# Optimization experiments

Hardware: AMD Instinct MI355X
Metric: run time of the kernel (lower is better)

The kernel has to match this reference:

```python
import jax, jax.numpy as jnp
import numpy as np

BITS = 4
GROUPSIZE = 128
IN_FEATURES = 4096
OUT_FEATURES = 11008
PACK = 32 // BITS  # 8 nibbles per int32
MASK = (1 << BITS) - 1


def setup_inputs() -> dict:
    key = jax.random.key(0)
    k1, k2, k3, k4, k5 = jax.random.split(key, 5)
    x = jax.random.normal(k1, (4, 2048, IN_FEATURES), dtype=jnp.float32)
    qweight = jax.random.randint(k2, (IN_FEATURES // 32 * BITS, OUT_FEATURES), 0, 2147483647, dtype=jnp.int32)
    n_groups = IN_FEATURES // GROUPSIZE  # 32
    qzeros = jax.random.randint(k3, (n_groups, OUT_FEATURES // 32 * BITS), 0, 2147483647, dtype=jnp.int32)
    scales = jax.random.uniform(k4, (n_groups, OUT_FEATURES), dtype=jnp.float32) * 0.01 + 1e-3
    bias = jax.random.normal(k5, (OUT_FEATURES,), dtype=jnp.float32)
    return {"x": x, "qweight": qweight, "qzeros": qzeros, "scales": scales, "bias": bias}


def _dequant(qweight, qzeros, scales):
    # GPTQ 4-bit unpack + group-wise dequant (g_idx=None / non-act-order path).
    shifts = jnp.arange(0, 32, BITS, dtype=jnp.int32)  # [8]
    # zero points: (G, out//8) int32 -> (G, out)
    z = ((qzeros[:, :, None] >> shifts[None, None, :]) & MASK)
    z = z.reshape(qzeros.shape[0], -1).astype(scales.dtype)  # (G, out)
    # weights: (in//8, out) int32 -> (in//8, 8, out) -> (G, groupsize, out)
    w = ((qweight[:, None, :] >> shifts[None, :, None]) & MASK).astype(scales.dtype)
    n_groups = scales.shape[0]
    w = w.reshape(n_groups, GROUPSIZE, -1)
    # W = scale * q - scale * zero, per group
    W = scales[:, None, :] * w - (z * scales)[:, None, :]
    return W.reshape(IN_FEATURES, OUT_FEATURES)


def reference(x, qweight, qzeros, scales, bias):
    W = _dequant(qweight, qzeros, scales)  # (in, out) fp32
    return jnp.matmul(x, W) + bias
```

## Files before the change

kernel.cpp:

```cpp
#include <hip/hip_runtime.h>
#include <hip/hip_bf16.h>
#include <stdint.h>

#define M_DIM 8192
#define K_DIM 4096
#define N_DIM 11008

typedef int i32x4 __attribute__((ext_vector_type(4)));
typedef float f32x4 __attribute__((ext_vector_type(4)));

typedef __attribute__((address_space(1))) const void global_cvoid;
typedef __attribute__((address_space(3))) void lds_void;

__device__ __forceinline__ void gload_lds16(const void* g, void* l) {
  __builtin_amdgcn_global_load_lds((global_cvoid*)g, (lds_void*)l, 16, 0, 0);
}

__global__ void k_prep(const float* __restrict__ x, signed char* __restrict__ xq,
                       float* __restrict__ sx, const int* __restrict__ qw,
                       const int* __restrict__ qz, signed char* __restrict__ wt) {
  if (blockIdx.x < M_DIM) {
    int m = blockIdx.x;
    int tx = threadIdx.x;
    const float4* row = (const float4*)(x + (size_t)m * K_DIM);
    float4 v[4];
    float mx = 0.f;
    #pragma unroll
    for (int i = 0; i < 4; ++i) {
      v[i] = row[tx * 4 + i];
      mx = fmaxf(mx, fmaxf(fmaxf(fabsf(v[i].x), fabsf(v[i].y)),
                           fmaxf(fabsf(v[i].z), fabsf(v[i].w))));
    }
    #pragma unroll
    for (int off = 1; off < 64; off <<= 1)
      mx = fmaxf(mx, __shfl_xor(mx, off));
    __shared__ float wmx[4];
    if ((tx & 63) == 0) wmx[tx >> 6] = mx;
    __syncthreads();
    mx = fmaxf(fmaxf(wmx[0], wmx[1]), fmaxf(wmx[2], wmx[3]));
    mx = fmaxf(mx, 1e-20f);
    float scale = 127.0f / mx;
    if (tx == 0) sx[m] = mx / 127.0f;
    union { signed char c[16]; uint4 u; } p;
    #pragma unroll
    for (int i = 0; i < 4; ++i) {
      p.c[i * 4 + 0] = (signed char)(int)rintf(v[i].x * scale);
      p.c[i * 4 + 1] = (signed char)(int)rintf(v[i].y * scale);
      p.c[i * 4 + 2] = (signed char)(int)rintf(v[i].z * scale);
      p.c[i * 4 + 3] = (signed char)(int)rintf(v[i].w * scale);
    }
    ((uint4*)(xq + (size_t)m * K_DIM))[tx] = p.u;
  } else {
    int b = blockIdx.x - M_DIM;
    int n = (b % 43) * 256 + threadIdx.x;
    int k8_0 = (b / 43) * 8;
    int g = (k8_0 * 8) >> 7;
    int zq = (qz[g * (N_DIM / 8) + (n >> 3)] >> ((n & 7) * 4)) & 15;
    #pragma unroll
    for (int i = 0; i < 8; ++i) {
      int k8 = k8_0 + i;
      int w = qw[(size_t)k8 * N_DIM + n];
      union { signed char c[8]; uint2 u; } r;
      #pragma unroll
      for (int j = 0; j < 8; ++j)
        r.c[j] = (signed char)(((w >> (4 * j)) & 15) - zq);
      *(uint2*)(wt + (size_t)n * K_DIM + (size_t)k8 * 8) = r.u;
    }
  }
}


#define MFMA_FIRST() do { \
  __builtin_amdgcn_s_setprio(1); \
  acci[0][0] = __builtin_amdgcn_mfma_i32_16x16x64_i8(af[0], bf[0], zq4, 0, 0, 0); \
  acci[0][1] = __builtin_amdgcn_mfma_i32_16x16x64_i8(af[0], bf[1], zq4, 0, 0, 0); \
  acci[0][2] = __builtin_amdgcn_mfma_i32_16x16x64_i8(af[0], bf[2], zq4, 0, 0, 0); \
  acci[0][3] = __builtin_amdgcn_mfma_i32_16x16x64_i8(af[0], bf[3], zq4, 0, 0, 0); \
  acci[1][0] = __builtin_amdgcn_mfma_i32_16x16x64_i8(af[1], bf[0], zq4, 0, 0, 0); \
  acci[1][1] = __builtin_amdgcn_mfma_i32_16x16x64_i8(af[1], bf[1], zq4, 0, 0, 0); \
  acci[1][2] = __builtin_amdgcn_mfma_i32_16x16x64_i8(af[1], bf[2], zq4, 0, 0, 0); \
  acci[1][3] = __builtin_amdgcn_mfma_i32_16x16x64_i8(af[1], bf[3], zq4, 0, 0, 0); \
  acci[2][0] = __builtin_amdgcn_mfma_i32_16x16x64_i8(af[2], bf[0], zq4, 0, 0, 0); \
  acci[2][1] = __builtin_amdgcn_mfma_i32_16x16x64_i8(af[2], bf[1], zq4, 0, 0, 0); \
  acci[2][2] = __builtin_amdgcn_mfma_i32_16x16x64_i8(af[2], bf[2], zq4, 0, 0, 0); \
  acci[2][3] = __builtin_amdgcn_mfma_i32_16x16x64_i8(af[2], bf[3], zq4, 0, 0, 0); \
  acci[3][0] = __builtin_amdgcn_mfma_i32_16x16x64_i8(af[3], bf[0], zq4, 0, 0, 0); \
  acci[3][1] = __builtin_amdgcn_mfma_i32_16x16x64_i8(af[3], bf[1], zq4, 0, 0, 0); \
  acci[3][2] = __builtin_amdgcn_mfma_i32_16x16x64_i8(af[3], bf[2], zq4, 0, 0, 0); \
  acci[3][3] = __builtin_amdgcn_mfma_i32_16x16x64_i8(af[3], bf[3], zq4, 0, 0, 0); \
  __builtin_amdgcn_s_setprio(0); \
} while (0)

#define MFMA_SECOND() do { \
  __builtin_amdgcn_s_setprio(1); \
  acci[0][0] = __builtin_amdgcn_mfma_i32_16x16x64_i8(af[0], bf[0], acci[0][0], 0, 0, 0); \
  acci[0][1] = __builtin_amdgcn_mfma_i32_16x16x64_i8(af[0], bf[1], acci[0][1], 0, 0, 0); \
  acci[0][2] = __builtin_amdgcn_mfma_i32_16x16x64_i8(af[0], bf[2], acci[0][2], 0, 0, 0); \
  acci[0][3] = __builtin_amdgcn_mfma_i32_16x16x64_i8(af[0], bf[3], acci[0][3], 0, 0, 0); \
  acci[1][0] = __builtin_amdgcn_mfma_i32_16x16x64_i8(af[1], bf[0], acci[1][0], 0, 0, 0); \
  acci[1][1] = __builtin_amdgcn_mfma_i32_16x16x64_i8(af[1], bf[1], acci[1][1], 0, 0, 0); \
  acci[1][2] = __builtin_amdgcn_mfma_i32_16x16x64_i8(af[1], bf[2], acci[1][2], 0, 0, 0); \
  acci[1][3] = __builtin_amdgcn_mfma_i32_16x16x64_i8(af[1], bf[3], acci[1][3], 0, 0, 0); \
  acci[2][0] = __builtin_amdgcn_mfma_i32_16x16x64_i8(af[2], bf[0], acci[2][0], 0, 0, 0); \
  acci[2][1] = __builtin_amdgcn_mfma_i32_16x16x64_i8(af[2], bf[1], acci[2][1], 0, 0, 0); \
  acci[2][2] = __builtin_amdgcn_mfma_i32_16x16x64_i8(af[2], bf[2], acci[2][2], 0, 0, 0); \
  acci[2][3] = __builtin_amdgcn_mfma_i32_16x16x64_i8(af[2], bf[3], acci[2][3], 0, 0, 0); \
  acci[3][0] = __builtin_amdgcn_mfma_i32_16x16x64_i8(af[3], bf[0], acci[3][0], 0, 0, 0); \
  acci[3][1] = __builtin_amdgcn_mfma_i32_16x16x64_i8(af[3], bf[1], acci[3][1], 0, 0, 0); \
  acci[3][2] = __builtin_amdgcn_mfma_i32_16x16x64_i8(af[3], bf[2], acci[3][2], 0, 0, 0); \
  acci[3][3] = __builtin_amdgcn_mfma_i32_16x16x64_i8(af[3], bf[3], acci[3][3], 0, 0, 0); \
  __builtin_amdgcn_s_setprio(0); \
} while (0)

#define LOADF(buf, ks) do { \
  const unsigned char* base_ = sh + (buf) * 32768; \
  af[0] = *(const i32x4*)(const void*)(base_ + (aoff0 ^ ((ks) << 6))); \
  af[1] = *(const i32x4*)(const void*)(base_ + (aoff1 ^ ((ks) << 6))); \
  af[2] = *(const i32x4*)(const void*)(base_ + (aoff2 ^ ((ks) << 6))); \
  af[3] = *(const i32x4*)(const void*)(base_ + (aoff3 ^ ((ks) << 6))); \
  bf[0] = *(const i32x4*)(const void*)(base_ + 16384 + (boff0 ^ ((ks) << 6))); \
  bf[1] = *(const i32x4*)(const void*)(base_ + 16384 + (boff1 ^ ((ks) << 6))); \
  bf[2] = *(const i32x4*)(const void*)(base_ + 16384 + (boff2 ^ ((ks) << 6))); \
  bf[3] = *(const i32x4*)(const void*)(base_ + 16384 + (boff3 ^ ((ks) << 6))); \
} while (0)

#define STAGE_ALL(buf, kt) do { \
  unsigned char* la_ = sh + (buf) * 32768 + w * 4096; \
  unsigned char* lb_ = la_ + 16384; \
  gload_lds16(pA + (kt) * 128, la_); \
  gload_lds16(pA + 8 * (size_t)K_DIM + (kt) * 128, la_ + 1024); \
  gload_lds16(pA + 16 * (size_t)K_DIM + (kt) * 128, la_ + 2048); \
  gload_lds16(pA + 24 * (size_t)K_DIM + (kt) * 128, la_ + 3072); \
  gload_lds16(pB + (kt) * 128, lb_); \
  gload_lds16(pB + 8 * (size_t)K_DIM + (kt) * 128, lb_ + 1024); \
  gload_lds16(pB + 16 * (size_t)K_DIM + (kt) * 128, lb_ + 2048); \
  gload_lds16(pB + 24 * (size_t)K_DIM + (kt) * 128, lb_ + 3072); \
} while (0)

#define WAIT_VM0 asm volatile("s_waitcnt vmcnt(0)" ::: "memory")
#define BAR() do { __builtin_amdgcn_s_barrier(); asm volatile("" ::: "memory"); } while (0)

__global__ __launch_bounds__(256, 2) void k_gemm8(const signed char* __restrict__ xq,
                                                  const signed char* __restrict__ wq,
                                                  const float* __restrict__ sc,
                                                  const float* __restrict__ sx,
                                                  const float* __restrict__ bias,
                                                  float* __restrict__ out) {
  __shared__ __align__(16) unsigned char sh[2 * 32768];

  const int nwg = gridDim.x;
  int bid = blockIdx.x;
  int swz = (bid & 7) * (nwg >> 3) + (bid >> 3);
  const int ntn = N_DIM / 128;
  int mt = swz / ntn;
  int nt = swz % ntn;

  const int tid = threadIdx.x;
  const int w = tid >> 6;
  const int lane = tid & 63;
  const int wm = w >> 1;
  const int wn = w & 1;
  const int fr = lane & 15;
  const int fq = lane >> 4;
  const int r7 = fr & 7;

  const int srow = lane >> 3;
  const int sslot = (lane & 7) ^ srow;
  const size_t goff = (size_t)srow * K_DIM + (size_t)sslot * 16;
  const signed char* pA = xq + (size_t)(mt * 128 + w * 32) * K_DIM + goff;
  const signed char* pB = wq + (size_t)(nt * 128 + w * 32) * K_DIM + goff;

  const int swb = (fq ^ r7) << 4;
  const int aoff0 = (wm * 64 + 0 * 16 + fr) * 128 + swb;
  const int aoff1 = (wm * 64 + 1 * 16 + fr) * 128 + swb;
  const int aoff2 = (wm * 64 + 2 * 16 + fr) * 128 + swb;
  const int aoff3 = (wm * 64 + 3 * 16 + fr) * 128 + swb;
  const int boff0 = (wn * 64 + 0 * 16 + fr) * 128 + swb;
  const int boff1 = (wn * 64 + 1 * 16 + fr) * 128 + swb;
  const int boff2 = (wn * 64 + 2 * 16 + fr) * 128 + swb;
  const int boff3 = (wn * 64 + 3 * 16 + fr) * 128 + swb;

  const int c0 = nt * 128 + wn * 64 + fr;

  i32x4 acci[4][4];
  f32x4 accf[4][4] = {};
  i32x4 af[4], bf[4];
  const i32x4 zq4 = {0, 0, 0, 0};

  STAGE_ALL(0, 0);
  WAIT_VM0;
  BAR();

  for (int t = 0; t < 32; ++t) {
    int buf = t & 1;
    if (t < 31) STAGE_ALL(buf ^ 1, t + 1);
    float sg0 = sc[(size_t)t * N_DIM + c0 + 0];
    float sg1 = sc[(size_t)t * N_DIM + c0 + 16];
    float sg2 = sc[(size_t)t * N_DIM + c0 + 32];
    float sg3 = sc[(size_t)t * N_DIM + c0 + 48];
    LOADF(buf, 0);
    MFMA_FIRST();
    LOADF(buf, 1);
    MFMA_SECOND();
    #pragma unroll
    for (int mi = 0; mi < 4; ++mi) {
      #pragma unroll
      for (int r = 0; r < 4; ++r) {
        accf[mi][0][r] += sg0 * (float)acci[mi][0][r];
        accf[mi][1][r] += sg1 * (float)acci[mi][1][r];
        accf[mi][2][r] += sg2 * (float)acci[mi][2][r];
        accf[mi][3][r] += sg3 * (float)acci[mi][3][r];
      }
    }
    WAIT_VM0;
    BAR();
  }

  const int r0 = mt * 128 + wm * 64 + fq * 4;
  #pragma unroll
  for (int mi = 0; mi < 4; ++mi) {
    float sxr[4];
    #pragma unroll
    for (int r = 0; r < 4; ++r) sxr[r] = sx[r0 + mi * 16 + r];
    #pragma unroll
    for (int nj = 0; nj < 4; ++nj) {
      int col = c0 + nj * 16;
      float bv = bias[col];
      size_t base = (size_t)(r0 + mi * 16) * N_DIM + col;
      #pragma unroll
      for (int r = 0; r < 4; ++r)
        out[base + (size_t)r * N_DIM] = sxr[r] * accf[mi][nj][r] + bv;
    }
  }
}

__global__ void k_fallback(const float* __restrict__ x, const int* __restrict__ qw,
                           const int* __restrict__ qz, const float* __restrict__ sc,
                           const float* __restrict__ bias, float* __restrict__ out) {
  int n = blockIdx.x * blockDim.x + threadIdx.x;
  int m = blockIdx.y;
  const float* xr = x + (size_t)m * K_DIM;
  float acc = 0.f;
  for (int g = 0; g < 32; ++g) {
    float s = sc[g * N_DIM + n];
    int zq = (qz[g * (N_DIM / 8) + (n >> 3)] >> ((n & 7) * 4)) & 15;
    float zs = s * (float)zq;
    for (int k8 = g * 16; k8 < g * 16 + 16; ++k8) {
      int w = qw[(size_t)k8 * N_DIM + n];
      #pragma unroll
      for (int j = 0; j < 8; ++j) {
        float wf = s * (float)((w >> (4 * j)) & 15) - zs;
        acc += wf * xr[k8 * 8 + j];
      }
    }
  }
  out[(size_t)m * N_DIM + n] = acc + bias[n];
}

extern "C" void kernel_launch(void* const* d_in, const int* in_sizes, int n_in,
                              void* d_out, int out_size, void* d_ws, size_t ws_size,
                              hipStream_t stream) {
  const float* x  = (const float*)d_in[0];
  const int* qw   = (const int*)d_in[1];
  const int* qz   = (const int*)d_in[2];
  const float* sc = (const float*)d_in[3];
  const float* bias = (const float*)d_in[4];
  float* out = (float*)d_out;

  const size_t xq_bytes = (size_t)M_DIM * K_DIM;
  const size_t sx_bytes = (size_t)M_DIM * sizeof(float);
  const size_t wq_bytes = (size_t)N_DIM * K_DIM;
  const size_t need = xq_bytes + sx_bytes + wq_bytes;

  if (ws_size >= need) {
    signed char* xq = (signed char*)d_ws;
    float* sx = (float*)((char*)d_ws + xq_bytes);
    signed char* wq = (signed char*)((char*)d_ws + xq_bytes + sx_bytes);
    k_prep<<<dim3(M_DIM + 2752), dim3(256), 0, stream>>>(x, xq, sx, qw, qz, wq);
    k_gemm8<<<dim3((M_DIM / 128) * (N_DIM / 128)), dim3(256), 0, stream>>>(xq, wq, sc, sx, bias, out);
  } else {
    k_fallback<<<dim3(N_DIM / 256, M_DIM), dim3(256), 0, stream>>>(x, qw, qz, sc, bias, out);
  }
}
```

Measured before the change: 574.6 us.

## Load B operand fragments directly from global memory instead of staging through LDS

The weight (B) tile is no longer copied into shared memory. Each wave reads its B fragments straight from global memory into registers, and only the activation (A) tile stays double-buffered in LDS. This halves LDS usage and removes LDS traffic for B, which could raise occupancy. The cost is that each B element is now fetched redundantly by the two waves that share it, and the global loads are exposed right before the MFMAs with little latency hiding. A single vmcnt(0) wait also mixes these loads with the A prefetch.

```diff
diff --git a/kernel.cpp b/kernel.cpp
--- a/kernel.cpp
+++ b/kernel.cpp
@@ -112,29 +112,28 @@
   __builtin_amdgcn_s_setprio(0); \
 } while (0)
 
-#define LOADF(buf, ks) do { \
-  const unsigned char* base_ = sh + (buf) * 32768; \
+#define LOADA_L(buf, ks) do { \
+  const unsigned char* base_ = sh + (buf) * 16384; \
   af[0] = *(const i32x4*)(const void*)(base_ + (aoff0 ^ ((ks) << 6))); \
   af[1] = *(const i32x4*)(const void*)(base_ + (aoff1 ^ ((ks) << 6))); \
   af[2] = *(const i32x4*)(const void*)(base_ + (aoff2 ^ ((ks) << 6))); \
   af[3] = *(const i32x4*)(const void*)(base_ + (aoff3 ^ ((ks) << 6))); \
-  bf[0] = *(const i32x4*)(const void*)(base_ + 16384 + (boff0 ^ ((ks) << 6))); \
-  bf[1] = *(const i32x4*)(const void*)(base_ + 16384 + (boff1 ^ ((ks) << 6))); \
-  bf[2] = *(const i32x4*)(const void*)(base_ + 16384 + (boff2 ^ ((ks) << 6))); \
-  bf[3] = *(const i32x4*)(const void*)(base_ + 16384 + (boff3 ^ ((ks) << 6))); \
-} while (0)
-
-#define STAGE_ALL(buf, kt) do { \
-  unsigned char* la_ = sh + (buf) * 32768 + w * 4096; \
-  unsigned char* lb_ = la_ + 16384; \
+} while (0)
+
+#define LOADB_G(t, ks) do { \
+  const signed char* b_ = pBg + (size_t)(t) * 128 + (ks) * 64; \
+  bf[0] = *(const i32x4*)(const void*)(b_); \
+  bf[1] = *(const i32x4*)(const void*)(b_ + 16 * (size_t)K_DIM); \
+  bf[2] = *(const i32x4*)(const void*)(b_ + 32 * (size_t)K_DIM); \
+  bf[3] = *(const i32x4*)(const void*)(b_ + 48 * (size_t)K_DIM); \
+} while (0)
+
+#define STAGE_A(buf, kt) do { \
+  unsigned char* la_ = sh + (buf) * 16384 + w * 4096; \
   gload_lds16(pA + (kt) * 128, la_); \
   gload_lds16(pA + 8 * (size_t)K_DIM + (kt) * 128, la_ + 1024); \
   gload_lds16(pA + 16 * (size_t)K_DIM + (kt) * 128, la_ + 2048); \
   gload_lds16(pA + 24 * (size_t)K_DIM + (kt) * 128, la_ + 3072); \
-  gload_lds16(pB + (kt) * 128, lb_); \
-  gload_lds16(pB + 8 * (size_t)K_DIM + (kt) * 128, lb_ + 1024); \
-  gload_lds16(pB + 16 * (size_t)K_DIM + (kt) * 128, lb_ + 2048); \
-  gload_lds16(pB + 24 * (size_t)K_DIM + (kt) * 128, lb_ + 3072); \
 } while (0)
 
 #define WAIT_VM0 asm volatile("s_waitcnt vmcnt(0)" ::: "memory")
@@ -146,7 +145,7 @@
                                                   const float* __restrict__ sx,
                                                   const float* __restrict__ bias,
                                                   float* __restrict__ out) {
-  __shared__ __align__(16) unsigned char sh[2 * 32768];
+  __shared__ __align__(16) unsigned char sh[2 * 16384];
 
   const int nwg = gridDim.x;
   int bid = blockIdx.x;
@@ -168,17 +167,14 @@
   const int sslot = (lane & 7) ^ srow;
   const size_t goff = (size_t)srow * K_DIM + (size_t)sslot * 16;
   const signed char* pA = xq + (size_t)(mt * 128 + w * 32) * K_DIM + goff;
-  const signed char* pB = wq + (size_t)(nt * 128 + w * 32) * K_DIM + goff;
+
+  const signed char* pBg = wq + (size_t)(nt * 128 + wn * 64 + fr) * K_DIM + fq * 16;
 
   const int swb = (fq ^ r7) << 4;
   const int aoff0 = (wm * 64 + 0 * 16 + fr) * 128 + swb;
   const int aoff1 = (wm * 64 + 1 * 16 + fr) * 128 + swb;
   const int aoff2 = (wm * 64 + 2 * 16 + fr) * 128 + swb;
   const int aoff3 = (wm * 64 + 3 * 16 + fr) * 128 + swb;
-  const int boff0 = (wn * 64 + 0 * 16 + fr) * 128 + swb;
-  const int boff1 = (wn * 64 + 1 * 16 + fr) * 128 + swb;
-  const int boff2 = (wn * 64 + 2 * 16 + fr) * 128 + swb;
-  const int boff3 = (wn * 64 + 3 * 16 + fr) * 128 + swb;
 
   const int c0 = nt * 128 + wn * 64 + fr;
 
@@ -187,20 +183,22 @@
   i32x4 af[4], bf[4];
   const i32x4 zq4 = {0, 0, 0, 0};
 
-  STAGE_ALL(0, 0);
+  STAGE_A(0, 0);
   WAIT_VM0;
   BAR();
 
   for (int t = 0; t < 32; ++t) {
     int buf = t & 1;
-    if (t < 31) STAGE_ALL(buf ^ 1, t + 1);
+    LOADB_G(t, 0);
+    if (t < 31) STAGE_A(buf ^ 1, t + 1);
     float sg0 = sc[(size_t)t * N_DIM + c0 + 0];
     float sg1 = sc[(size_t)t * N_DIM + c0 + 16];
     float sg2 = sc[(size_t)t * N_DIM + c0 + 32];
     float sg3 = sc[(size_t)t * N_DIM + c0 + 48];
-    LOADF(buf, 0);
+    LOADA_L(buf, 0);
     MFMA_FIRST();
-    LOADF(buf, 1);
+    LOADB_G(t, 1);
+    LOADA_L(buf, 1);
     MFMA_SECOND();
     #pragma unroll
     for (int mi = 0; mi < 4; ++mi) {
```

New measurement: 917.2 us. 1.6x slower.
